# Performance work log

Measured on AMD Instinct MI355X. Metric: run time of the kernel, lower is better.

## Reference

```python
import jax, jax.numpy as jnp
import numpy as np

B, HQ, HK, S, D, HID, BS = 2, 32, 8, 8192, 128, 128, 16
NB = S // BS  # 512 pooled blocks


def rotate_half(x):
    h = x.shape[-1] // 2
    return jnp.concatenate([-x[..., h:], x[..., :h]], axis=-1)


def pool_cat(x):
    # avg + max pooling over block_size along the sequence dim, concat on feature dim
    b, h, s, d = x.shape
    xb = x.reshape(b, h, s // BS, BS, d)
    return jnp.concatenate([xb.mean(axis=3), xb.max(axis=3)], axis=-1)  # [b,h,NB,2d]


def setup_inputs() -> dict:
    key = jax.random.key(0)
    k0, k1, k2, k3 = jax.random.split(key, 4)
    q = jax.random.normal(k0, (B, HQ, S, D), jnp.float32)
    k = jax.random.normal(k1, (B, HK, S, D), jnp.float32)
    wq = jax.random.normal(k2, (HQ, 2 * D, HID), jnp.float32) / np.float32(np.sqrt(2 * D))
    wk = jax.random.normal(k3, (HK, 2 * D, HID), jnp.float32) / np.float32(np.sqrt(2 * D))
    # causal block mask
    mask = jnp.broadcast_to(jnp.tril(jnp.ones((NB, NB), bool))[None, None], (B, 1, NB, NB))
    # RoPE tables over pooled positions
    pos = jnp.arange(NB, dtype=jnp.float32)
    inv_freq = 1.0 / (10000.0 ** (jnp.arange(0, HID, 2, dtype=jnp.float32) / HID))
    freqs = pos[:, None] * inv_freq[None, :]              # [NB, HID/2]
    emb = jnp.concatenate([freqs, freqs], axis=-1)        # [NB, HID]
    cos = jnp.broadcast_to(jnp.cos(emb)[None], (B, NB, HID))
    sin = jnp.broadcast_to(jnp.sin(emb)[None], (B, NB, HID))
    return {"q": q, "k": k, "attention_mask": mask, "cos": cos, "sin": sin, "wq": wq, "wk": wk}


def reference(q, k, attention_mask, cos, sin, wq, wk):
    # pooled multi-head linear projections
    qh = jnp.einsum('bhnc,hcd->bhnd', pool_cat(q), wq)   # [B,HQ,NB,HID]
    kh = jnp.einsum('bhnc,hcd->bhnd', pool_cat(k), wk)   # [B,HK,NB,HID]
    # RoPE (unsqueeze_dim=1)
    c, s = cos[:, None], sin[:, None]
    qh = qh * c + rotate_half(qh) * s
    kh = kh * c + rotate_half(kh) * s
    # GQA: repeat kv heads
    kh = jnp.repeat(kh, HQ // HK, axis=1)                # [B,HQ,NB,HID]
    attn = jnp.einsum('bhqd,bhkd->bhqk', qh, kh) / jnp.sqrt(jnp.float32(HID))
    attn = jnp.where(attention_mask, attn, jnp.float32(-1e9))
    return jax.nn.softmax(attn, axis=-1)
```

## Files before the change

kernel.cpp:

```cpp
#include <hip/hip_runtime.h>

namespace {
constexpr int BB  = 2;
constexpr int HQ  = 32;
constexpr int HK  = 8;
constexpr int S   = 8192;
constexpr int D   = 128;
constexpr int HID = 128;
constexpr int BS  = 16;
constexpr int NB  = 512;
constexpr int C2D = 256;
constexpr int RW  = 256;
constexpr int WTR = 512;
}

typedef __attribute__((ext_vector_type(8))) short short8;
typedef __attribute__((ext_vector_type(4))) float f32x4;

__device__ inline unsigned short f2bf(float f) {
  unsigned u = __builtin_bit_cast(unsigned, f);
  unsigned r = u + 0x7fff + ((u >> 16) & 1);
  return (unsigned short)(r >> 16);
}
__device__ inline float bf2f(unsigned short s) {
  unsigned u = ((unsigned)s) << 16;
  return __builtin_bit_cast(float, u);
}

__global__ __launch_bounds__(256) void wprep_kernel(
    const float* __restrict__ wq, const float* __restrict__ wk,
    unsigned short* __restrict__ wT)
{
  __shared__ float ts[32 * 33];
  const int t  = threadIdx.x;
  const int kc = blockIdx.x;
  const int hy = blockIdx.y;
  const float* w = (hy < HQ) ? (wq + (size_t)hy * C2D * HID)
                             : (wk + (size_t)(hy - HQ) * C2D * HID);
  for (int nc = 0; nc < 4; ++nc) {
    __syncthreads();
    {
      const int r = t >> 3, c4 = t & 7;
      *(float4*)&ts[r * 33 + 4 * c4] =
          *(const float4*)(w + (size_t)(kc * 32 + r) * HID + nc * 32 + 4 * c4);
    }
    __syncthreads();
    {
      const int n = t >> 3, g = t & 7;
      const int cb = 8 * (g & 3);
      short8 v;
#pragma unroll
      for (int j = 0; j < 8; ++j) {
        const float f = ts[(cb + j) * 33 + n];
        const unsigned short h = f2bf(f);
        v[j] = (short)((g < 4) ? h : f2bf(f - bf2f(h)));
      }
      unsigned short* dst = wT + ((size_t)hy * HID + nc * 32 + n) * WTR +
                            ((g < 4) ? 0 : 256) + kc * 32 + cb;
      *(short8*)dst = v;
    }
  }
}

__global__ __launch_bounds__(256) void pool_gemm_rope_kernel(
    const float* __restrict__ qx, const float* __restrict__ kx,
    const unsigned short* __restrict__ wT,
    const float* __restrict__ cosp, const float* __restrict__ sinp,
    unsigned short* __restrict__ qhb, unsigned short* __restrict__ khb)
{
  constexpr int AST = 520;
  constexpr int CST = 132;
  __shared__ unsigned short As[32 * AST];
  float* Cs = (float*)As;

  const int t  = threadIdx.x;
  const int n0 = blockIdx.x * 32;
  const int hy = blockIdx.y;
  const int b  = blockIdx.z;

  const float* x; unsigned short* o; int H; int h; bool isq;
  if (hy < HQ) { x = qx; o = qhb; H = HQ; h = hy; isq = true; }
  else         { x = kx; o = khb; H = HK; h = hy - HQ; isq = false; }

  const float* xb = x + (((size_t)b * H + h) * S + (size_t)n0 * BS) * D;
  for (int it = t; it < 32 * 32; it += 256) {
    const int m = it >> 5, d4 = it & 31;
    const float4* p = (const float4*)(xb + (size_t)m * BS * D) + d4;
    float4 v = p[0];
    float sx = v.x, sy = v.y, sz = v.z, sw = v.w;
    float mx = v.x, my = v.y, mz = v.z, mw = v.w;
#pragma unroll
    for (int i = 1; i < BS; ++i) {
      v = p[i * (D / 4)];
      sx += v.x; sy += v.y; sz += v.z; sw += v.w;
      mx = fmaxf(mx, v.x); my = fmaxf(my, v.y);
      mz = fmaxf(mz, v.z); mw = fmaxf(mw, v.w);
    }
    const float inv16 = 1.0f / 16.0f;
    float mn[4] = {sx * inv16, sy * inv16, sz * inv16, sw * inv16};
    float mv[4] = {mx, my, mz, mw};
    ushort4 mh, ml, xh, xl;
    mh.x = f2bf(mn[0]); ml.x = f2bf(mn[0] - bf2f(mh.x));
    mh.y = f2bf(mn[1]); ml.y = f2bf(mn[1] - bf2f(mh.y));
    mh.z = f2bf(mn[2]); ml.z = f2bf(mn[2] - bf2f(mh.z));
    mh.w = f2bf(mn[3]); ml.w = f2bf(mn[3] - bf2f(mh.w));
    xh.x = f2bf(mv[0]); xl.x = f2bf(mv[0] - bf2f(xh.x));
    xh.y = f2bf(mv[1]); xl.y = f2bf(mv[1] - bf2f(xh.y));
    xh.z = f2bf(mv[2]); xl.z = f2bf(mv[2] - bf2f(xh.z));
    xh.w = f2bf(mv[3]); xl.w = f2bf(mv[3] - bf2f(xh.w));
    unsigned short* row = &As[m * AST];
    *(ushort4*)(row + 4 * d4)       = mh;
    *(ushort4*)(row + 256 + 4 * d4) = ml;
    *(ushort4*)(row + 128 + 4 * d4) = xh;
    *(ushort4*)(row + 384 + 4 * d4) = xl;
  }
  __syncthreads();

  const int w    = t >> 6;
  const int lane = t & 63;
  const int col  = lane & 15;
  const int quad = lane >> 4;
  const int mtile = w & 1;
  const int nbase = (w >> 1) * 64;

  const unsigned short* arow = &As[(size_t)(mtile * 16 + col) * AST + quad * 8];
  const unsigned short* bp = wT + ((size_t)hy * HID + nbase + col) * WTR + quad * 8;

  f32x4 acc[4];
#pragma unroll
  for (int i = 0; i < 4; ++i) acc[i] = (f32x4){0.f, 0.f, 0.f, 0.f};

#pragma unroll
  for (int ks = 0; ks < 8; ++ks) {
    const short8 ahi = *(const short8*)(arow + ks * 32);
    const short8 alo = *(const short8*)(arow + 256 + ks * 32);
#pragma unroll
    for (int nt = 0; nt < 4; ++nt) {
      const short8 bhi = *(const short8*)(bp + (size_t)nt * 16 * WTR + ks * 32);
      const short8 blo = *(const short8*)(bp + (size_t)nt * 16 * WTR + 256 + ks * 32);
      acc[nt] = __builtin_amdgcn_mfma_f32_16x16x32_bf16(ahi, bhi, acc[nt], 0, 0, 0);
      acc[nt] = __builtin_amdgcn_mfma_f32_16x16x32_bf16(ahi, blo, acc[nt], 0, 0, 0);
      acc[nt] = __builtin_amdgcn_mfma_f32_16x16x32_bf16(alo, bhi, acc[nt], 0, 0, 0);
    }
  }
  __syncthreads();

#pragma unroll
  for (int nt = 0; nt < 4; ++nt)
#pragma unroll
    for (int r = 0; r < 4; ++r)
      Cs[(size_t)(mtile * 16 + quad * 4 + r) * CST + nbase + nt * 16 + col] =
          acc[nt][r];
  __syncthreads();

  const int dt = t & 31, mt = t >> 5;
  const int d0 = dt * 4, m0 = mt * 4;
  const float sgn = (d0 < 64) ? -1.0f : 1.0f;
  const float qscale = isq ? 0.08838834764831843f : 1.0f;
#pragma unroll
  for (int i = 0; i < 4; ++i) {
    const int n = n0 + m0 + i;
    const float4 cv = *(const float4*)(cosp + ((size_t)b * NB + n) * HID + d0);
    const float4 sv = *(const float4*)(sinp + ((size_t)b * NB + n) * HID + d0);
    const float4 cur = *(const float4*)&Cs[(m0 + i) * CST + d0];
    const float4 pr  = *(const float4*)&Cs[(m0 + i) * CST + (d0 ^ 64)];
    float ov[4];
    ov[0] = (cur.x * cv.x + sgn * pr.x * sv.x) * qscale;
    ov[1] = (cur.y * cv.y + sgn * pr.y * sv.y) * qscale;
    ov[2] = (cur.z * cv.z + sgn * pr.z * sv.z) * qscale;
    ov[3] = (cur.w * cv.w + sgn * pr.w * sv.w) * qscale;
    ushort4 hi, lo;
    hi.x = f2bf(ov[0]); lo.x = f2bf(ov[0] - bf2f(hi.x));
    hi.y = f2bf(ov[1]); lo.y = f2bf(ov[1] - bf2f(hi.y));
    hi.z = f2bf(ov[2]); lo.z = f2bf(ov[2] - bf2f(hi.z));
    hi.w = f2bf(ov[3]); lo.w = f2bf(ov[3] - bf2f(hi.w));
    unsigned short* orow = o + (((size_t)b * H + h) * NB + n) * RW + d0;
    *(ushort4*)orow = hi;
    *(ushort4*)(orow + 128) = lo;
  }
}

__global__ __launch_bounds__(256) void attn_kernel(
    const unsigned short* __restrict__ qhb,
    const unsigned short* __restrict__ khb,
    float* __restrict__ out)
{
  __shared__ float rs_lds[16];

  const int t = threadIdx.x;
  const int w = t >> 6;
  const int lane = t & 63;
  const int col = lane & 15;
  const int quad = lane >> 4;
  const int x = blockIdx.x;
  const int h = blockIdx.y;
  const int b = blockIdx.z;

  const unsigned short* qbase = qhb + (((size_t)b * HQ + h) * NB) * RW;
  const unsigned short* kbase = khb + (((size_t)b * HK + (h >> 2)) * NB) * RW;
  float* obase = out + (((size_t)b * HQ + h) * NB) * (size_t)NB;

  for (int ph = 0; ph < 2; ++ph) {
    const int strip = ph ? (31 - x) : x;

    __syncthreads();
    if (t < 16) rs_lds[t] = 0.f;
    __syncthreads();

    const unsigned short* qrow = qbase + (size_t)(strip * 16 + col) * RW + quad * 8;
    short8 qf[8];
#pragma unroll
    for (int f = 0; f < 4; ++f) {
      qf[f]     = *(const short8*)(qrow + f * 32);
      qf[4 + f] = *(const short8*)(qrow + f * 32 + 128);
    }

    const unsigned short* krow = kbase + (size_t)col * RW + quad * 8;
    const int n = (w <= strip) ? ((strip - w) >> 2) + 1 : 0;

    f32x4 pbuf[8];
    float rs[4] = {0.f, 0.f, 0.f, 0.f};

#pragma unroll
    for (int ti = 0; ti < 8; ++ti) {
      if (ti < n) {
        const int k16 = w + 4 * ti;
        const unsigned short* kr = krow + (size_t)k16 * 16 * RW;
        short8 kf[8];
#pragma unroll
        for (int f = 0; f < 4; ++f) {
          kf[f]     = *(const short8*)(kr + f * 32);
          kf[4 + f] = *(const short8*)(kr + f * 32 + 128);
        }
        f32x4 acc = {0.f, 0.f, 0.f, 0.f};
#pragma unroll
        for (int f = 0; f < 4; ++f) {
          acc = __builtin_amdgcn_mfma_f32_16x16x32_bf16(qf[f],     kf[f],     acc, 0, 0, 0);
          acc = __builtin_amdgcn_mfma_f32_16x16x32_bf16(qf[f],     kf[4 + f], acc, 0, 0, 0);
          acc = __builtin_amdgcn_mfma_f32_16x16x32_bf16(qf[4 + f], kf[f],     acc, 0, 0, 0);
        }
        const bool diag = (k16 == strip);
        f32x4 p;
#pragma unroll
        for (int r = 0; r < 4; ++r) {
          float v = __expf(acc[r]);
          if (diag && col > quad * 4 + r) v = 0.f;
          p[r] = v;
          rs[r] += v;
        }
        pbuf[ti] = p;
      }
    }

#pragma unroll
    for (int r = 0; r < 4; ++r) {
      float v = rs[r];
      v += __shfl_xor(v, 1, 64);
      v += __shfl_xor(v, 2, 64);
      v += __shfl_xor(v, 4, 64);
      v += __shfl_xor(v, 8, 64);
      if (col == 0) atomicAdd(&rs_lds[quad * 4 + r], v);
    }

    {
      const int r = t & 15;
      const float4 z = make_float4(0.f, 0.f, 0.f, 0.f);
      for (int c4 = (strip + 1) * 4 + (t >> 4); c4 < 128; c4 += 16)
        *(float4*)(obase + (size_t)(strip * 16 + r) * NB + 4 * c4) = z;
    }

    __syncthreads();

    float inv[4];
#pragma unroll
    for (int r = 0; r < 4; ++r) inv[r] = 1.0f / rs_lds[quad * 4 + r];

#pragma unroll
    for (int ti = 0; ti < 8; ++ti) {
      if (ti < n) {
        const int k16 = w + 4 * ti;
#pragma unroll
        for (int r = 0; r < 4; ++r)
          obase[(size_t)(strip * 16 + quad * 4 + r) * NB + k16 * 16 + col] =
              pbuf[ti][r] * inv[r];
      }
    }
  }
}

extern "C" void kernel_launch(void* const* d_in, const int* in_sizes, int n_in,
                              void* d_out, int out_size, void* d_ws, size_t ws_size,
                              hipStream_t stream)
{
  const float* q    = (const float*)d_in[0];
  const float* k    = (const float*)d_in[1];
  const float* cosp = (const float*)d_in[3];
  const float* sinp = (const float*)d_in[4];
  const float* wq   = (const float*)d_in[5];
  const float* wk   = (const float*)d_in[6];
  float* out = (float*)d_out;

  unsigned short* qhb = (unsigned short*)d_ws;
  unsigned short* khb = qhb + (size_t)BB * HQ * NB * RW;
  unsigned short* wTp = khb + (size_t)BB * HK * NB * RW;

  hipLaunchKernelGGL(wprep_kernel, dim3(8, HQ + HK), dim3(256),
                     0, stream, wq, wk, wTp);
  hipLaunchKernelGGL(pool_gemm_rope_kernel, dim3(NB / 32, HQ + HK, BB), dim3(256),
                     0, stream, q, k, wTp, cosp, sinp, qhb, khb);
  hipLaunchKernelGGL(attn_kernel, dim3(16, HQ, BB), dim3(256),
                     0, stream, qhb, khb, out);
}
```

Baseline: 480.3 us.

## Store projected Q/K in MFMA fragment order and simplify attention grid

```diff
diff --git a/kernel.cpp b/kernel.cpp
--- a/kernel.cpp
+++ b/kernel.cpp
@@ -10,8 +10,8 @@
 constexpr int BS  = 16;
 constexpr int NB  = 512;
 constexpr int C2D = 256;
-constexpr int RW  = 256;
 constexpr int WTR = 512;
+constexpr int BLK = 4096;
 }
 
 typedef __attribute__((ext_vector_type(8))) short short8;
@@ -157,6 +157,7 @@
   const int d0 = dt * 4, m0 = mt * 4;
   const float sgn = (d0 < 64) ? -1.0f : 1.0f;
   const float qscale = isq ? 0.08838834764831843f : 1.0f;
+  float4 ov[4];
 #pragma unroll
   for (int i = 0; i < 4; ++i) {
     const int n = n0 + m0 + i;
@@ -164,19 +165,41 @@
     const float4 sv = *(const float4*)(sinp + ((size_t)b * NB + n) * HID + d0);
     const float4 cur = *(const float4*)&Cs[(m0 + i) * CST + d0];
     const float4 pr  = *(const float4*)&Cs[(m0 + i) * CST + (d0 ^ 64)];
-    float ov[4];
-    ov[0] = (cur.x * cv.x + sgn * pr.x * sv.x) * qscale;
-    ov[1] = (cur.y * cv.y + sgn * pr.y * sv.y) * qscale;
-    ov[2] = (cur.z * cv.z + sgn * pr.z * sv.z) * qscale;
-    ov[3] = (cur.w * cv.w + sgn * pr.w * sv.w) * qscale;
-    ushort4 hi, lo;
-    hi.x = f2bf(ov[0]); lo.x = f2bf(ov[0] - bf2f(hi.x));
-    hi.y = f2bf(ov[1]); lo.y = f2bf(ov[1] - bf2f(hi.y));
-    hi.z = f2bf(ov[2]); lo.z = f2bf(ov[2] - bf2f(hi.z));
-    hi.w = f2bf(ov[3]); lo.w = f2bf(ov[3] - bf2f(hi.w));
-    unsigned short* orow = o + (((size_t)b * H + h) * NB + n) * RW + d0;
-    *(ushort4*)orow = hi;
-    *(ushort4*)(orow + 128) = lo;
+    ov[i].x = (cur.x * cv.x + sgn * pr.x * sv.x) * qscale;
+    ov[i].y = (cur.y * cv.y + sgn * pr.y * sv.y) * qscale;
+    ov[i].z = (cur.z * cv.z + sgn * pr.z * sv.z) * qscale;
+    ov[i].w = (cur.w * cv.w + sgn * pr.w * sv.w) * qscale;
+  }
+  __syncthreads();
+#pragma unroll
+  for (int i = 0; i < 4; ++i)
+    *(float4*)&Cs[(m0 + i) * CST + d0] = ov[i];
+  __syncthreads();
+
+  unsigned short* obase = o + ((size_t)b * H + h) * (size_t)(32 * BLK) +
+                          (size_t)(n0 >> 4) * BLK;
+#pragma unroll
+  for (int j = 0; j < 4; ++j) {
+    const int c = t + 256 * j;
+    const int k16c = c >> 9;
+    const int fi   = (c >> 6) & 7;
+    const int ln   = c & 63;
+    const int colr = ln & 15, quadr = ln >> 4;
+    const int n = k16c * 16 + colr;
+    const int dstart = (fi & 3) * 32 + quadr * 8;
+    const float* src = &Cs[n * CST + dstart];
+    short8 outv;
+    if (fi < 4) {
+#pragma unroll
+      for (int e = 0; e < 8; ++e) outv[e] = (short)f2bf(src[e]);
+    } else {
+#pragma unroll
+      for (int e = 0; e < 8; ++e) {
+        const float f = src[e];
+        outv[e] = (short)f2bf(f - bf2f(f2bf(f)));
+      }
+    }
+    *(short8*)(obase + (size_t)k16c * BLK + (fi * 64 + ln) * 8) = outv;
   }
 }
 
@@ -192,98 +215,89 @@
   const int lane = t & 63;
   const int col = lane & 15;
   const int quad = lane >> 4;
-  const int x = blockIdx.x;
+  const int strip = blockIdx.x;
   const int h = blockIdx.y;
   const int b = blockIdx.z;
 
-  const unsigned short* qbase = qhb + (((size_t)b * HQ + h) * NB) * RW;
-  const unsigned short* kbase = khb + (((size_t)b * HK + (h >> 2)) * NB) * RW;
+  const unsigned short* qfb = qhb + (((size_t)b * HQ + h) * 32 + strip) * BLK;
+  const unsigned short* kfb = khb + (((size_t)b * HK + (h >> 2)) * 32) * BLK;
   float* obase = out + (((size_t)b * HQ + h) * NB) * (size_t)NB;
 
-  for (int ph = 0; ph < 2; ++ph) {
-    const int strip = ph ? (31 - x) : x;
-
-    __syncthreads();
-    if (t < 16) rs_lds[t] = 0.f;
-    __syncthreads();
-
-    const unsigned short* qrow = qbase + (size_t)(strip * 16 + col) * RW + quad * 8;
-    short8 qf[8];
-#pragma unroll
-    for (int f = 0; f < 4; ++f) {
-      qf[f]     = *(const short8*)(qrow + f * 32);
-      qf[4 + f] = *(const short8*)(qrow + f * 32 + 128);
-    }
-
-    const unsigned short* krow = kbase + (size_t)col * RW + quad * 8;
-    const int n = (w <= strip) ? ((strip - w) >> 2) + 1 : 0;
-
-    f32x4 pbuf[8];
-    float rs[4] = {0.f, 0.f, 0.f, 0.f};
-
-#pragma unroll
-    for (int ti = 0; ti < 8; ++ti) {
-      if (ti < n) {
-        const int k16 = w + 4 * ti;
-        const unsigned short* kr = krow + (size_t)k16 * 16 * RW;
-        short8 kf[8];
-#pragma unroll
-        for (int f = 0; f < 4; ++f) {
-          kf[f]     = *(const short8*)(kr + f * 32);
-          kf[4 + f] = *(const short8*)(kr + f * 32 + 128);
-        }
-        f32x4 acc = {0.f, 0.f, 0.f, 0.f};
-#pragma unroll
-        for (int f = 0; f < 4; ++f) {
-          acc = __builtin_amdgcn_mfma_f32_16x16x32_bf16(qf[f],     kf[f],     acc, 0, 0, 0);
-          acc = __builtin_amdgcn_mfma_f32_16x16x32_bf16(qf[f],     kf[4 + f], acc, 0, 0, 0);
-          acc = __builtin_amdgcn_mfma_f32_16x16x32_bf16(qf[4 + f], kf[f],     acc, 0, 0, 0);
-        }
-        const bool diag = (k16 == strip);
-        f32x4 p;
-#pragma unroll
-        for (int r = 0; r < 4; ++r) {
-          float v = __expf(acc[r]);
-          if (diag && col > quad * 4 + r) v = 0.f;
-          p[r] = v;
-          rs[r] += v;
-        }
-        pbuf[ti] = p;
+  if (t < 16) rs_lds[t] = 0.f;
+  __syncthreads();
+
+  short8 qf[8];
+#pragma unroll
+  for (int fi = 0; fi < 8; ++fi)
+    qf[fi] = *(const short8*)(qfb + (fi * 64 + lane) * 8);
+
+  const int n = (w <= strip) ? ((strip - w) >> 2) + 1 : 0;
+
+  f32x4 pbuf[8];
+  float rs[4] = {0.f, 0.f, 0.f, 0.f};
+
+#pragma unroll
+  for (int ti = 0; ti < 8; ++ti) {
+    if (ti < n) {
+      const int k16 = w + 4 * ti;
+      const unsigned short* kp = kfb + (size_t)k16 * BLK + lane * 8;
+      short8 kf[8];
+#pragma unroll
+      for (int fi = 0; fi < 8; ++fi)
+        kf[fi] = *(const short8*)(kp + fi * 512);
+      f32x4 accA = {0.f, 0.f, 0.f, 0.f};
+      f32x4 accB = {0.f, 0.f, 0.f, 0.f};
+      f32x4 accC = {0.f, 0.f, 0.f, 0.f};
+#pragma unroll
+      for (int f = 0; f < 4; ++f) {
+        accA = __builtin_amdgcn_mfma_f32_16x16x32_bf16(qf[f],     kf[f],     accA, 0, 0, 0);
+        accB = __builtin_amdgcn_mfma_f32_16x16x32_bf16(qf[f],     kf[4 + f], accB, 0, 0, 0);
+        accC = __builtin_amdgcn_mfma_f32_16x16x32_bf16(qf[4 + f], kf[f],     accC, 0, 0, 0);
       }
-    }
-
-#pragma unroll
-    for (int r = 0; r < 4; ++r) {
-      float v = rs[r];
-      v += __shfl_xor(v, 1, 64);
-      v += __shfl_xor(v, 2, 64);
-      v += __shfl_xor(v, 4, 64);
-      v += __shfl_xor(v, 8, 64);
-      if (col == 0) atomicAdd(&rs_lds[quad * 4 + r], v);
-    }
-
-    {
-      const int r = t & 15;
-      const float4 z = make_float4(0.f, 0.f, 0.f, 0.f);
-      for (int c4 = (strip + 1) * 4 + (t >> 4); c4 < 128; c4 += 16)
-        *(float4*)(obase + (size_t)(strip * 16 + r) * NB + 4 * c4) = z;
-    }
-
-    __syncthreads();
-
-    float inv[4];
-#pragma unroll
-    for (int r = 0; r < 4; ++r) inv[r] = 1.0f / rs_lds[quad * 4 + r];
-
-#pragma unroll
-    for (int ti = 0; ti < 8; ++ti) {
-      if (ti < n) {
-        const int k16 = w + 4 * ti;
-#pragma unroll
-        for (int r = 0; r < 4; ++r)
-          obase[(size_t)(strip * 16 + quad * 4 + r) * NB + k16 * 16 + col] =
-              pbuf[ti][r] * inv[r];
+      const bool diag = (k16 == strip);
+      f32x4 p;
+#pragma unroll
+      for (int r = 0; r < 4; ++r) {
+        float v = __expf(accA[r] + accB[r] + accC[r]);
+        if (diag && col > quad * 4 + r) v = 0.f;
+        p[r] = v;
+        rs[r] += v;
       }
+      pbuf[ti] = p;
+    }
+  }
+
+#pragma unroll
+  for (int r = 0; r < 4; ++r) {
+    float v = rs[r];
+    v += __shfl_xor(v, 1, 64);
+    v += __shfl_xor(v, 2, 64);
+    v += __shfl_xor(v, 4, 64);
+    v += __shfl_xor(v, 8, 64);
+    if (col == 0) atomicAdd(&rs_lds[quad * 4 + r], v);
+  }
+
+  {
+    const int r = t >> 4;
+    const float4 z = make_float4(0.f, 0.f, 0.f, 0.f);
+    for (int c4 = (strip + 1) * 4 + (t & 15); c4 < 128; c4 += 16)
+      *(float4*)(obase + (size_t)(strip * 16 + r) * NB + 4 * c4) = z;
+  }
+
+  __syncthreads();
+
+  float inv[4];
+#pragma unroll
+  for (int r = 0; r < 4; ++r) inv[r] = 1.0f / rs_lds[quad * 4 + r];
+
+#pragma unroll
+  for (int ti = 0; ti < 8; ++ti) {
+    if (ti < n) {
+      const int k16 = w + 4 * ti;
+#pragma unroll
+      for (int r = 0; r < 4; ++r)
+        obase[(size_t)(strip * 16 + quad * 4 + r) * NB + k16 * 16 + col] =
+            pbuf[ti][r] * inv[r];
     }
   }
 }
@@ -301,13 +315,13 @@
   float* out = (float*)d_out;
 
   unsigned short* qhb = (unsigned short*)d_ws;
-  unsigned short* khb = qhb + (size_t)BB * HQ * NB * RW;
-  unsigned short* wTp = khb + (size_t)BB * HK * NB * RW;
+  unsigned short* khb = qhb + (size_t)BB * HQ * 32 * BLK;
+  unsigned short* wTp = khb + (size_t)BB * HK * 32 * BLK;
 
   hipLaunchKernelGGL(wprep_kernel, dim3(8, HQ + HK), dim3(256),
                      0, stream, wq, wk, wTp);
   hipLaunchKernelGGL(pool_gemm_rope_kernel, dim3(NB / 32, HQ + HK, BB), dim3(256),
                      0, stream, q, k, wTp, cosp, sinp, qhb, khb);
-  hipLaunchKernelGGL(attn_kernel, dim3(16, HQ, BB), dim3(256),
+  hipLaunchKernelGGL(attn_kernel, dim3(32, HQ, BB), dim3(256),
                      0, stream, qhb, khb, out);
 }
```

After: 469.2 us. -2.3%, faster.
